# Performance work log

Measured on AMD Instinct MI355X. Metric: run time of the kernel, lower is better.

## Reference

```python
import jax, jax.numpy as jnp
import numpy as np

NUM_EMBEDDINGS = 1024
EMBEDDING_DIM = 64
COMMITMENT_COST = 0.25


def setup_inputs() -> dict:
    key = jax.random.key(0)
    k1, k2 = jax.random.split(key)
    inputs = jax.random.normal(k1, (64, 32, 32, EMBEDDING_DIM), dtype=jnp.float32)
    # torch init is uniform(-1/K, 1/K); scale accordingly
    weight = jax.random.uniform(
        k2, (NUM_EMBEDDINGS, EMBEDDING_DIM), dtype=jnp.float32,
        minval=-1.0 / NUM_EMBEDDINGS, maxval=1.0 / NUM_EMBEDDINGS)
    return {"inputs": inputs, "weight": weight}


def reference(inputs, weight):
    input_shape = inputs.shape
    flat = inputs.reshape(-1, EMBEDDING_DIM)               # [N, D]
    distances = (jnp.sum(flat ** 2, axis=1, keepdims=True)
                 + jnp.sum(weight ** 2, axis=1)
                 - 2.0 * flat @ weight.T)                   # [N, K]
    encoding_indices = jnp.argmin(distances, axis=1)        # [N]
    # gather codes (equivalent to one-hot @ weight, but as a direct gather)
    quantized = weight[encoding_indices].reshape(input_shape)

    e_latent_loss = jnp.mean((jax.lax.stop_gradient(quantized) - inputs) ** 2)
    q_latent_loss = jnp.mean((quantized - jax.lax.stop_gradient(inputs)) ** 2)
    loss = q_latent_loss + COMMITMENT_COST * e_latent_loss

    # straight-through estimator
    quantized_ste = inputs + jax.lax.stop_gradient(quantized - inputs)

    # perplexity (equivalent to mean over the one-hot encodings)
    n_tokens = flat.shape[0]
    counts = jax.ops.segment_sum(
        jnp.ones((n_tokens,), jnp.float32), encoding_indices,
        num_segments=NUM_EMBEDDINGS)
    avg_probs = counts / n_tokens
    perplexity = jnp.exp(-jnp.sum(avg_probs * jnp.log(avg_probs + 1e-10)))

    indices_for_transformer = encoding_indices.reshape(input_shape[0], -1)
    return (loss, quantized_ste, perplexity, indices_for_transformer)
```

## Files before the change

### kernel.cpp

```cpp
#include <hip/hip_runtime.h>
#include <cstdint>
#include <cstddef>

#define N_TOKENS 65536
#define DIM 64
#define K_CODES 1024
#define NTH 256
#define NTHM 512
#define TPB 128
#define NCH 16
#define NBLK (N_TOKENS / TPB)

#define OFF_Q 1
#define OFF_PERP 4194305
#define OFF_IDX 4194306

#define MARGIN 1.5e-4f
#define HMARGIN 7.5e-5f

#define WS_LOSS   0
#define WS_TICKET 8
#define WS_COUNTS 16
#define WS_WHI    4112
#define WS_WLO    135184
#define WS_S2     266256

typedef __attribute__((ext_vector_type(8))) short  s16x8;
typedef __attribute__((ext_vector_type(4))) float  f32x4;

__device__ __forceinline__ float fmulr(float a, float b){ return __fmul_rn(a,b); }
__device__ __forceinline__ float faddr(float a, float b){ return __fadd_rn(a,b); }

__device__ __forceinline__ unsigned short f2bf(float f) {
    unsigned u = __float_as_uint(f);
    unsigned r = u + 0x7fffu + ((u >> 16) & 1u);
    return (unsigned short)(r >> 16);
}
__device__ __forceinline__ float bf2f(unsigned short h) {
    return __uint_as_float(((unsigned)h) << 16);
}

__device__ float sumsq64_np(const float* __restrict__ p) {
    float s[16];
    #pragma unroll
    for (int l = 0; l < 16; ++l) {
        float a0 = fmulr(p[l],      p[l]);
        float a1 = fmulr(p[l + 16], p[l + 16]);
        float a2 = fmulr(p[l + 32], p[l + 32]);
        float a3 = fmulr(p[l + 48], p[l + 48]);
        s[l] = faddr(faddr(a0, a1), faddr(a2, a3));
    }
    #pragma unroll
    for (int len = 8; len >= 1; len >>= 1)
        #pragma unroll
        for (int l = 0; l < len; ++l)
            s[l] = faddr(s[l], s[l + len]);
    return s[0];
}

__device__ __forceinline__ void async_copy16(const void* g, void* l) {
    __builtin_amdgcn_global_load_lds(
        (const __attribute__((address_space(1))) void*)g,
        (__attribute__((address_space(3))) void*)l, 16, 0, 0);
}

__global__ void vq_prep(const float* __restrict__ W, unsigned short* __restrict__ Whi,
                        unsigned short* __restrict__ Wlo, float* __restrict__ s2g,
                        int* __restrict__ counts, int* __restrict__ ticket,
                        double* __restrict__ loss_acc) {
    int gid = blockIdx.x * NTH + threadIdx.x;
    for (int e = gid; e < K_CODES * DIM; e += 16384) {
        float x = W[e];
        unsigned short hi = f2bf(x);
        unsigned short lo = f2bf(__fsub_rn(x, bf2f(hi)));
        int j = e >> 6, k = e & 63;
        int pos = j * 64 + (((k >> 3) ^ (j & 7)) << 3) + (k & 7);
        Whi[pos] = hi; Wlo[pos] = lo;
    }
    if (gid < K_CODES) { s2g[gid] = sumsq64_np(W + gid * 64); counts[gid] = 0; }
    if (gid == 0) { *loss_acc = 0.0; *ticket = 0; }
}

__device__ void final_scalars(int* __restrict__ counts, double* __restrict__ loss_acc,
                              float* __restrict__ out, int tid, double* hred) {
    double h = 0.0;
    for (int j = tid; j < K_CODES; j += NTHM) {
        int cj = atomicAdd(&counts[j], 0);
        double p = (double)cj / 65536.0;
        h += p * log(p + 1e-10);
    }
    #pragma unroll
    for (int off = 32; off >= 1; off >>= 1) h += __shfl_down(h, off, 64);
    if ((tid & 63) == 0) hred[tid >> 6] = h;
    __syncthreads();
    if (tid == 0) {
        double H = 0.0;
        #pragma unroll
        for (int w = 0; w < 8; ++w) H += hred[w];
        out[OFF_PERP] = (float)exp(-H);
        double ls = atomicAdd(loss_acc, 0.0);
        float Lf = (float)(ls / 4194304.0);
        out[0] = faddr(Lf, fmulr(0.25f, Lf));
    }
}

__global__ __launch_bounds__(NTHM, 4)
void vq_main(const float* __restrict__ X, const float* __restrict__ W,
             const unsigned short* __restrict__ WhiG, const unsigned short* __restrict__ WloG,
             const float* __restrict__ s2g, float* __restrict__ out,
             double* __restrict__ loss_acc, int* __restrict__ counts,
             int* __restrict__ ticket) {
    __shared__ __align__(16) char U[32768];
    __shared__ __align__(16) float s2s[K_CODES];
    __shared__ int fcount, lastflag;
    __shared__ double lred[8];

    unsigned short* xs_hi = (unsigned short*)U;
    unsigned short* xs_lo = (unsigned short*)(U + 16384);
    unsigned* maskL = (unsigned*)U;
    float (*sm1)[TPB] = (float (*)[TPB])(U + 16384);
    float (*sm2)[TPB] = (float (*)[TPB])(U + 17408);
    int   (*si1)[TPB] = (int   (*)[TPB])(U + 18432);
    int*   fidx  = (int*)(U + 19456);
    int*   flist = (int*)(U + 19968);
    float* s1f   = (float*)(U + 20480);

    const int tid  = threadIdx.x;
    const int lane = tid & 63, wave = tid >> 6;
    const int quad = lane >> 4, lrow = lane & 15;
    const int tg   = wave & 3;
    const int chd  = wave >> 2;
    const int t0   = blockIdx.x * TPB;

    if (tid == 0) fcount = 0;

    if (tid < 256) *(f32x4*)&s2s[tid * 4] = *(const f32x4*)&s2g[tid * 4];
    #pragma unroll
    for (int i = 0; i < 2; ++i) {
        int g = tid + NTHM * i;
        int t = g >> 3, kb = g & 7;
        const float* src = X + (size_t)(t0 + t) * DIM + kb * 8;
        float v[8];
        *(f32x4*)v       = *(const f32x4*)src;
        *(f32x4*)(v + 4) = *(const f32x4*)(src + 4);
        unsigned short h[8], l[8];
        #pragma unroll
        for (int k = 0; k < 8; ++k) {
            h[k] = f2bf(v[k]);
            l[k] = f2bf(__fsub_rn(v[k], bf2f(h[k])));
        }
        int base = t * 64 + ((kb ^ (t & 7)) << 3);
        *(s16x8*)&xs_hi[base] = *(s16x8*)h;
        *(s16x8*)&xs_lo[base] = *(s16x8*)l;
    }
    __syncthreads();

    s16x8 a_h0[2], a_h1[2], a_l0[2], a_l1[2];
    #pragma unroll
    for (int rt = 0; rt < 2; ++rt) {
        int tf = tg * 32 + rt * 16 + lrow;
        int sA = tf & 7;
        a_h0[rt] = *(const s16x8*)&xs_hi[tf * 64 + (((0 + quad) ^ sA) << 3)];
        a_h1[rt] = *(const s16x8*)&xs_hi[tf * 64 + (((4 + quad) ^ sA) << 3)];
        a_l0[rt] = *(const s16x8*)&xs_lo[tf * 64 + (((0 + quad) ^ sA) << 3)];
        a_l1[rt] = *(const s16x8*)&xs_lo[tf * 64 + (((4 + quad) ^ sA) << 3)];
    }
    __syncthreads();

    {
        const char* gh = (const char*)WhiG;
        const char* gl = (const char*)WloG;
        async_copy16(gh + tid * 16, U + wave * 1024);
        async_copy16(gl + tid * 16, U + 16384 + wave * 1024);
    }
    __syncthreads();

    float m1v[8], m2v[8]; int m1i[8]; unsigned cmask[8];
    #pragma unroll
    for (int ri = 0; ri < 8; ++ri) {
        m1v[ri] = -3.4e38f; m2v[ri] = -3.4e38f; m1i[ri] = 0x7fffffff; cmask[ri] = 0u;
    }

    for (int ch = 0; ch < NCH; ++ch) {
        const int buf = ch & 1;
        if (ch < NCH - 1) {
            const char* gh = (const char*)WhiG + (ch + 1) * 8192;
            const char* gl = (const char*)WloG + (ch + 1) * 8192;
            async_copy16(gh + tid * 16, U + (buf ^ 1) * 8192 + wave * 1024);
            async_copy16(gl + tid * 16, U + 16384 + (buf ^ 1) * 8192 + wave * 1024);
        }
        const unsigned short* wh = (const unsigned short*)(U + buf * 8192);
        const unsigned short* wl = (const unsigned short*)(U + 16384 + buf * 8192);
        #pragma unroll
        for (int ct2 = 0; ct2 < 2; ++ct2) {
            int lc = chd * 32 + ct2 * 16 + lrow;
            int sB = lrow & 7;
            const unsigned short* bh = &wh[lc * 64];
            const unsigned short* bl = &wl[lc * 64];
            s16x8 b_h0 = *(const s16x8*)&bh[((0 + quad) ^ sB) << 3];
            s16x8 b_h1 = *(const s16x8*)&bh[((4 + quad) ^ sB) << 3];
            s16x8 b_l0 = *(const s16x8*)&bl[((0 + quad) ^ sB) << 3];
            s16x8 b_l1 = *(const s16x8*)&bl[((4 + quad) ^ sB) << 3];
            int jcode = ch * 64 + lc;
            float s2v = s2s[jcode];
            float ainit = fmulr(-0.5f, s2v);
            #pragma unroll
            for (int rt = 0; rt < 2; ++rt) {
                f32x4 acc = {ainit, ainit, ainit, ainit};
                acc = __builtin_amdgcn_mfma_f32_16x16x32_bf16(a_h0[rt], b_h0, acc, 0, 0, 0);
                acc = __builtin_amdgcn_mfma_f32_16x16x32_bf16(a_h1[rt], b_h1, acc, 0, 0, 0);
                acc = __builtin_amdgcn_mfma_f32_16x16x32_bf16(a_h0[rt], b_l0, acc, 0, 0, 0);
                acc = __builtin_amdgcn_mfma_f32_16x16x32_bf16(a_h1[rt], b_l1, acc, 0, 0, 0);
                acc = __builtin_amdgcn_mfma_f32_16x16x32_bf16(a_l0[rt], b_h0, acc, 0, 0, 0);
                acc = __builtin_amdgcn_mfma_f32_16x16x32_bf16(a_l1[rt], b_h1, acc, 0, 0, 0);
                #pragma unroll
                for (int r = 0; r < 4; ++r) {
                    float a = acc[r];
                    int ri = rt * 4 + r;
                    float thr = m1v[ri];
                    bool gt = a > thr;
                    float sec = gt ? thr : a;
                    m2v[ri] = fmaxf(m2v[ri], sec);
                    m1v[ri] = gt ? a : thr;
                    m1i[ri] = gt ? jcode : m1i[ri];
                    unsigned cnd = (faddr(a, HMARGIN) > thr) ? 1u : 0u;
                    cmask[ri] = cmask[ri] * 2u + cnd;
                }
            }
        }
        __syncthreads();
    }

    {
        unsigned* mrow = maskL + (wave * 64 + lane) * 8;
        #pragma unroll
        for (int ri = 0; ri < 8; ++ri) mrow[ri] = cmask[ri];
    }

    #pragma unroll
    for (int m = 1; m <= 8; m <<= 1) {
        #pragma unroll
        for (int ri = 0; ri < 8; ++ri) {
            float o1v = __shfl_xor(m1v[ri], m, 64);
            int   o1i = __shfl_xor(m1i[ri], m, 64);
            float o2v = __shfl_xor(m2v[ri], m, 64);
            bool take = (o1v > m1v[ri]) || (o1v == m1v[ri] && o1i < m1i[ri]);
            float loser = take ? m1v[ri] : o1v;
            m2v[ri] = fmaxf(fmaxf(m2v[ri], o2v), loser);
            if (take) { m1v[ri] = o1v; m1i[ri] = o1i; }
        }
    }
    if (lrow == 0) {
        #pragma unroll
        for (int ri = 0; ri < 8; ++ri) {
            int rt = ri >> 2, r = ri & 3;
            int t = tg * 32 + rt * 16 + quad * 4 + r;
            sm1[chd][t] = m1v[ri];
            sm2[chd][t] = m2v[ri];
            si1[chd][t] = m1i[ri];
        }
    }
    __syncthreads();
    if (tid < TPB) {
        int t = tid;
        float a1 = sm1[0][t], b1 = sm1[1][t];
        int   ia = si1[0][t], ib = si1[1][t];
        float a2 = sm2[0][t], b2 = sm2[1][t];
        bool take = (b1 > a1) || (b1 == a1 && ib < ia);
        float w1 = take ? b1 : a1;
        int   wi = take ? ib : ia;
        float loser = take ? a1 : b1;
        float w2 = fmaxf(fmaxf(a2, b2), loser);
        bool fb = __fsub_rn(w1, w2) < HMARGIN;
        fidx[t] = fb ? (wi | (int)0x80000000) : wi;
        if (fb) { int p = atomicAdd(&fcount, 1); flist[p] = t; }
    }
    __syncthreads();

    const int fc = fcount;
    if (tid < fc) s1f[tid] = sumsq64_np(X + (size_t)(t0 + flist[tid]) * 64);

    double lsum = 0.0;
    #pragma unroll
    for (int i = 0; i < 4; ++i) {
        int e4 = tid + NTHM * i;
        int t = e4 >> 4, d4 = (e4 & 15) * 4;
        int iv = fidx[t];
        if (iv >= 0) {
            f32x4 q = *(const f32x4*)&W[iv * 64 + d4];
            f32x4 x = *(const f32x4*)&X[(size_t)(t0 + t) * 64 + d4];
            *(f32x4*)&out[(size_t)OFF_Q + (size_t)(t0 + t) * 64 + d4] = q;
            #pragma unroll
            for (int c = 0; c < 4; ++c) {
                float df = __fsub_rn(q[c], x[c]);
                lsum += (double)fmulr(df, df);
            }
        }
    }
    if (tid < TPB) {
        int iv = fidx[tid];
        if (iv >= 0) {
            atomicAdd(&counts[iv], 1);
            out[(size_t)OFF_IDX + t0 + tid] = (float)iv;
        }
    }
    __syncthreads();

    for (int ti = wave; ti < fc; ti += 8) {
        int t = flist[ti];
        int tok = t0 + t;
        unsigned long long best = ~0ULL;
        if (lane < 32) {
            int chd_ = lane >> 4, lr_ = lane & 15;
            int tg_ = t >> 5, rt_ = (t >> 4) & 1, quad_ = (t >> 2) & 3, r_ = t & 3;
            unsigned msk = maskL[((chd_ * 4 + tg_) * 64 + quad_ * 16 + lr_) * 8
                                 + rt_ * 4 + r_];
            const float* xr = X + (size_t)tok * 64;
            float s1 = s1f[ti];
            while (msk) {
                int p = __builtin_ctz(msk);
                msk &= msk - 1u;
                int q = 31 - p;
                int j = (q >> 1) * 64 + chd_ * 32 + ((q & 1) << 4) + lr_;
                const float* wr = W + (size_t)j * 64;
                float acc = 0.0f;
                #pragma unroll
                for (int kb = 0; kb < 16; ++kb) {
                    f32x4 xv = *(const f32x4*)(xr + kb * 4);
                    f32x4 wv = *(const f32x4*)(wr + kb * 4);
                    acc = __builtin_fmaf(xv[0], wv[0], acc);
                    acc = __builtin_fmaf(xv[1], wv[1], acc);
                    acc = __builtin_fmaf(xv[2], wv[2], acc);
                    acc = __builtin_fmaf(xv[3], wv[3], acc);
                }
                float d = faddr(faddr(s1, s2s[j]), fmulr(-2.0f, acc));
                unsigned long long pk =
                    ((unsigned long long)__float_as_uint(d) << 32) |
                    (unsigned long long)(unsigned)j;
                best = (pk < best) ? pk : best;
            }
        }
        #pragma unroll
        for (int m = 32; m >= 1; m >>= 1) {
            unsigned long long o =
                ((unsigned long long)(unsigned)__shfl_xor((int)(best >> 32), m, 64) << 32) |
                (unsigned long long)(unsigned)__shfl_xor((int)(best & 0xffffffffu), m, 64);
            best = (o < best) ? o : best;
        }
        if (lane == 0) {
            int idx = (int)(best & 0xffffffffu);
            fidx[t] = idx;
            out[(size_t)OFF_IDX + tok] = (float)idx;
            atomicAdd(&counts[idx], 1);
        }
    }
    __syncthreads();

    for (int g = tid; g < fc * 16; g += NTHM) {
        int ti = g >> 4, d4 = (g & 15) * 4;
        int t = flist[ti];
        int idx = fidx[t];
        f32x4 q = *(const f32x4*)&W[idx * 64 + d4];
        f32x4 x = *(const f32x4*)&X[(size_t)(t0 + t) * 64 + d4];
        *(f32x4*)&out[(size_t)OFF_Q + (size_t)(t0 + t) * 64 + d4] = q;
        #pragma unroll
        for (int c = 0; c < 4; ++c) {
            float df = __fsub_rn(q[c], x[c]);
            lsum += (double)fmulr(df, df);
        }
    }

    #pragma unroll
    for (int off = 32; off >= 1; off >>= 1) lsum += __shfl_down(lsum, off, 64);
    if (lane == 0) lred[wave] = lsum;
    __syncthreads();
    if (tid == 0) {
        double s = 0.0;
        #pragma unroll
        for (int w = 0; w < 8; ++w) s += lred[w];
        atomicAdd(loss_acc, s);
    }
    __threadfence();
    __syncthreads();
    if (tid == 0) lastflag = (atomicAdd(ticket, 1) == NBLK - 1);
    __syncthreads();
    if (lastflag) {
        __threadfence();
        final_scalars(counts, loss_acc, out, tid, lred);
    }
}

extern "C" void kernel_launch(void* const* d_in, const int* in_sizes, int n_in,
                              void* d_out, int out_size, void* d_ws, size_t ws_size,
                              hipStream_t stream) {
    const float* X = (const float*)d_in[0];
    const float* W = (const float*)d_in[1];
    float* out = (float*)d_out;
    char* ws = (char*)d_ws;
    double* loss_acc = (double*)(ws + WS_LOSS);
    int* ticket = (int*)(ws + WS_TICKET);
    int* counts = (int*)(ws + WS_COUNTS);
    unsigned short* Whi = (unsigned short*)(ws + WS_WHI);
    unsigned short* Wlo = (unsigned short*)(ws + WS_WLO);
    float* s2g = (float*)(ws + WS_S2);

    vq_prep<<<64, NTH, 0, stream>>>(W, Whi, Wlo, s2g, counts, ticket, loss_acc);
    vq_main<<<NBLK, NTHM, 0, stream>>>(X, W, Whi, Wlo, s2g, out,
                                       loss_acc, counts, ticket);
}
```

Baseline: 195.5 us.

## Resolve near-tie tokens in registers with LDS atomicMin, drop mask staging

The kernel now gives the X tiles, the W double buffers and the reduction arrays separate shared-memory buffers instead of aliasing one union. Because of that, the first W chunk's async copy can start before X is staged, and two barriers go away. The fallback exact-distance recheck for ambiguous tokens now runs directly from each thread's candidate-mask registers and merges results with shared 64-bit atomicMin. This replaces writing masks to LDS and a per-wave loop with shuffle reductions. The costs are higher LDS use, which may lower occupancy, and candidate work that is now spread unevenly across lanes.

```diff
diff --git a/kernel.cpp b/kernel.cpp
--- a/kernel.cpp
+++ b/kernel.cpp
@@ -110,20 +110,20 @@
              const float* __restrict__ s2g, float* __restrict__ out,
              double* __restrict__ loss_acc, int* __restrict__ counts,
              int* __restrict__ ticket) {
-    __shared__ __align__(16) char U[32768];
+    __shared__ __align__(16) unsigned short xs_hi[TPB * 64];
+    __shared__ __align__(16) unsigned short xs_lo[TPB * 64];
+    __shared__ __align__(16) unsigned short ws_hi[2][64 * 64];
+    __shared__ __align__(16) unsigned short ws_lo[2][64 * 64];
     __shared__ __align__(16) float s2s[K_CODES];
+    __shared__ float sm1[2][TPB];
+    __shared__ float sm2[2][TPB];
+    __shared__ int   si1[2][TPB];
+    __shared__ int fidx[TPB];
+    __shared__ int flist[TPB];
+    __shared__ float s1f[TPB];
+    __shared__ unsigned long long tbest[TPB];
     __shared__ int fcount, lastflag;
     __shared__ double lred[8];
-
-    unsigned short* xs_hi = (unsigned short*)U;
-    unsigned short* xs_lo = (unsigned short*)(U + 16384);
-    unsigned* maskL = (unsigned*)U;
-    float (*sm1)[TPB] = (float (*)[TPB])(U + 16384);
-    float (*sm2)[TPB] = (float (*)[TPB])(U + 17408);
-    int   (*si1)[TPB] = (int   (*)[TPB])(U + 18432);
-    int*   fidx  = (int*)(U + 19456);
-    int*   flist = (int*)(U + 19968);
-    float* s1f   = (float*)(U + 20480);
 
     const int tid  = threadIdx.x;
     const int lane = tid & 63, wave = tid >> 6;
@@ -134,6 +134,14 @@
 
     if (tid == 0) fcount = 0;
 
+    {
+        const char* gh = (const char*)WhiG;
+        const char* gl = (const char*)WloG;
+        char* lh = (char*)&ws_hi[0][0] + wave * 1024;
+        char* ll = (char*)&ws_lo[0][0] + wave * 1024;
+        async_copy16(gh + tid * 16, lh);
+        async_copy16(gl + tid * 16, ll);
+    }
     if (tid < 256) *(f32x4*)&s2s[tid * 4] = *(const f32x4*)&s2g[tid * 4];
     #pragma unroll
     for (int i = 0; i < 2; ++i) {
@@ -165,15 +173,6 @@
         a_l0[rt] = *(const s16x8*)&xs_lo[tf * 64 + (((0 + quad) ^ sA) << 3)];
         a_l1[rt] = *(const s16x8*)&xs_lo[tf * 64 + (((4 + quad) ^ sA) << 3)];
     }
-    __syncthreads();
-
-    {
-        const char* gh = (const char*)WhiG;
-        const char* gl = (const char*)WloG;
-        async_copy16(gh + tid * 16, U + wave * 1024);
-        async_copy16(gl + tid * 16, U + 16384 + wave * 1024);
-    }
-    __syncthreads();
 
     float m1v[8], m2v[8]; int m1i[8]; unsigned cmask[8];
     #pragma unroll
@@ -186,17 +185,17 @@
         if (ch < NCH - 1) {
             const char* gh = (const char*)WhiG + (ch + 1) * 8192;
             const char* gl = (const char*)WloG + (ch + 1) * 8192;
-            async_copy16(gh + tid * 16, U + (buf ^ 1) * 8192 + wave * 1024);
-            async_copy16(gl + tid * 16, U + 16384 + (buf ^ 1) * 8192 + wave * 1024);
-        }
-        const unsigned short* wh = (const unsigned short*)(U + buf * 8192);
-        const unsigned short* wl = (const unsigned short*)(U + 16384 + buf * 8192);
+            char* lh = (char*)&ws_hi[buf ^ 1][0] + wave * 1024;
+            char* ll = (char*)&ws_lo[buf ^ 1][0] + wave * 1024;
+            async_copy16(gh + tid * 16, lh);
+            async_copy16(gl + tid * 16, ll);
+        }
         #pragma unroll
         for (int ct2 = 0; ct2 < 2; ++ct2) {
             int lc = chd * 32 + ct2 * 16 + lrow;
             int sB = lrow & 7;
-            const unsigned short* bh = &wh[lc * 64];
-            const unsigned short* bl = &wl[lc * 64];
+            const unsigned short* bh = &ws_hi[buf][lc * 64];
+            const unsigned short* bl = &ws_lo[buf][lc * 64];
             s16x8 b_h0 = *(const s16x8*)&bh[((0 + quad) ^ sB) << 3];
             s16x8 b_h1 = *(const s16x8*)&bh[((4 + quad) ^ sB) << 3];
             s16x8 b_l0 = *(const s16x8*)&bl[((0 + quad) ^ sB) << 3];
@@ -223,18 +222,12 @@
                     m2v[ri] = fmaxf(m2v[ri], sec);
                     m1v[ri] = gt ? a : thr;
                     m1i[ri] = gt ? jcode : m1i[ri];
-                    unsigned cnd = (faddr(a, HMARGIN) > thr) ? 1u : 0u;
-                    cmask[ri] = cmask[ri] * 2u + cnd;
+                    cmask[ri] = cmask[ri] * 2u +
+                                ((faddr(a, HMARGIN) > thr) ? 1u : 0u);
                 }
             }
         }
         __syncthreads();
-    }
-
-    {
-        unsigned* mrow = maskL + (wave * 64 + lane) * 8;
-        #pragma unroll
-        for (int ri = 0; ri < 8; ++ri) mrow[ri] = cmask[ri];
     }
 
     #pragma unroll
@@ -263,6 +256,7 @@
     __syncthreads();
     if (tid < TPB) {
         int t = tid;
+        tbest[t] = ~0ULL;
         float a1 = sm1[0][t], b1 = sm1[1][t];
         int   ia = si1[0][t], ib = si1[1][t];
         float a2 = sm2[0][t], b2 = sm2[1][t];
@@ -273,12 +267,45 @@
         float w2 = fmaxf(fmaxf(a2, b2), loser);
         bool fb = __fsub_rn(w1, w2) < HMARGIN;
         fidx[t] = fb ? (wi | (int)0x80000000) : wi;
-        if (fb) { int p = atomicAdd(&fcount, 1); flist[p] = t; }
-    }
-    __syncthreads();
-
-    const int fc = fcount;
-    if (tid < fc) s1f[tid] = sumsq64_np(X + (size_t)(t0 + flist[tid]) * 64);
+        if (fb) {
+            int p = atomicAdd(&fcount, 1);
+            flist[p] = t;
+            s1f[t] = sumsq64_np(X + (size_t)(t0 + t) * 64);
+        }
+    }
+    __syncthreads();
+
+    #pragma unroll
+    for (int ri = 0; ri < 8; ++ri) {
+        int rt = ri >> 2, r = ri & 3;
+        int t = tg * 32 + rt * 16 + quad * 4 + r;
+        if (fidx[t] >= 0) continue;
+        unsigned msk = cmask[ri];
+        const float* xr = X + (size_t)(t0 + t) * 64;
+        float s1 = s1f[t];
+        while (msk) {
+            int p = __builtin_ctz(msk);
+            msk &= msk - 1u;
+            int q = 31 - p;
+            int j = (q >> 1) * 64 + chd * 32 + ((q & 1) << 4) + lrow;
+            const float* wr = W + (size_t)j * 64;
+            float acc = 0.0f;
+            #pragma unroll
+            for (int kb = 0; kb < 16; ++kb) {
+                f32x4 xv = *(const f32x4*)(xr + kb * 4);
+                f32x4 wv = *(const f32x4*)(wr + kb * 4);
+                acc = __builtin_fmaf(xv[0], wv[0], acc);
+                acc = __builtin_fmaf(xv[1], wv[1], acc);
+                acc = __builtin_fmaf(xv[2], wv[2], acc);
+                acc = __builtin_fmaf(xv[3], wv[3], acc);
+            }
+            float d = faddr(faddr(s1, s2s[j]), fmulr(-2.0f, acc));
+            unsigned long long pk =
+                ((unsigned long long)__float_as_uint(d) << 32) |
+                (unsigned long long)(unsigned)j;
+            atomicMin(&tbest[t], pk);
+        }
+    }
 
     double lsum = 0.0;
     #pragma unroll
@@ -306,56 +333,15 @@
     }
     __syncthreads();
 
-    for (int ti = wave; ti < fc; ti += 8) {
-        int t = flist[ti];
-        int tok = t0 + t;
-        unsigned long long best = ~0ULL;
-        if (lane < 32) {
-            int chd_ = lane >> 4, lr_ = lane & 15;
-            int tg_ = t >> 5, rt_ = (t >> 4) & 1, quad_ = (t >> 2) & 3, r_ = t & 3;
-            unsigned msk = maskL[((chd_ * 4 + tg_) * 64 + quad_ * 16 + lr_) * 8
-                                 + rt_ * 4 + r_];
-            const float* xr = X + (size_t)tok * 64;
-            float s1 = s1f[ti];
-            while (msk) {
-                int p = __builtin_ctz(msk);
-                msk &= msk - 1u;
-                int q = 31 - p;
-                int j = (q >> 1) * 64 + chd_ * 32 + ((q & 1) << 4) + lr_;
-                const float* wr = W + (size_t)j * 64;
-                float acc = 0.0f;
-                #pragma unroll
-                for (int kb = 0; kb < 16; ++kb) {
-                    f32x4 xv = *(const f32x4*)(xr + kb * 4);
-                    f32x4 wv = *(const f32x4*)(wr + kb * 4);
-                    acc = __builtin_fmaf(xv[0], wv[0], acc);
-                    acc = __builtin_fmaf(xv[1], wv[1], acc);
-                    acc = __builtin_fmaf(xv[2], wv[2], acc);
-                    acc = __builtin_fmaf(xv[3], wv[3], acc);
-                }
-                float d = faddr(faddr(s1, s2s[j]), fmulr(-2.0f, acc));
-                unsigned long long pk =
-                    ((unsigned long long)__float_as_uint(d) << 32) |
-                    (unsigned long long)(unsigned)j;
-                best = (pk < best) ? pk : best;
-            }
-        }
-        #pragma unroll
-        for (int m = 32; m >= 1; m >>= 1) {
-            unsigned long long o =
-                ((unsigned long long)(unsigned)__shfl_xor((int)(best >> 32), m, 64) << 32) |
-                (unsigned long long)(unsigned)__shfl_xor((int)(best & 0xffffffffu), m, 64);
-            best = (o < best) ? o : best;
-        }
-        if (lane == 0) {
-            int idx = (int)(best & 0xffffffffu);
-            fidx[t] = idx;
-            out[(size_t)OFF_IDX + tok] = (float)idx;
-            atomicAdd(&counts[idx], 1);
-        }
-    }
-    __syncthreads();
-
+    if (tid < TPB && fidx[tid] < 0) {
+        int idx = (int)(tbest[tid] & 0xffffffffu);
+        fidx[tid] = idx;
+        out[(size_t)OFF_IDX + t0 + tid] = (float)idx;
+        atomicAdd(&counts[idx], 1);
+    }
+    __syncthreads();
+
+    const int fc = fcount;
     for (int g = tid; g < fc * 16; g += NTHM) {
         int ti = g >> 4, d4 = (g & 15) * 4;
         int t = flist[ti];
```

New measurement: 235.7 us. +20.6%, slower.
